# Performance work log

Hardware: AMD Instinct MI355X
Metric: run time of the kernel (lower is better)

The kernel has to match this reference:

```python
import jax, jax.numpy as jnp
import numpy as np

D = 256          # out_feats
H = 4            # n_heads
DH = D // H      # per-head feats
S = 8192         # number of snapshots (segments)
PER = 32         # edges (selected papers) per snapshot
E = S * PER      # total edges
NP = 200000      # number of papers
ST = 10          # snapshot_types (embedding has ST+1 rows, padding_idx=-1)
SLOPE = 0.01     # LeakyReLU negative slope (torch default)


def setup_inputs() -> dict:
    key = jax.random.key(0)
    ks = jax.random.split(key, 20)
    sc = 1.0 / np.sqrt(D)
    papers = jax.random.normal(ks[0], (NP, D), dtype=jnp.float32)
    snapshots = jax.random.normal(ks[1], (S, D), dtype=jnp.float32)
    cur_snapshot_types = jax.random.randint(ks[2], (S,), 0, ST + 1, dtype=jnp.int32)
    is_cite = jax.random.randint(ks[3], (NP,), 0, 2, dtype=jnp.int32)
    selected_indicator = jax.random.randint(ks[4], (E,), 0, NP, dtype=jnp.int64)
    # contiguous sorted segment ids, PER edges per snapshot (matches valid_num_nodes)
    index = jnp.repeat(jnp.arange(S, dtype=jnp.int32), PER)
    # linear layers (torch Linear: y = x @ W.T + b)
    W_src = jax.random.normal(ks[5], (D, D), dtype=jnp.float32) * sc
    b_src = jnp.zeros((D,), dtype=jnp.float32)
    W_dst = jax.random.normal(ks[6], (D, D), dtype=jnp.float32) * sc
    b_dst = jnp.zeros((D,), dtype=jnp.float32)
    W_out = jax.random.normal(ks[7], (D, D), dtype=jnp.float32) * sc
    b_out = jnp.zeros((D,), dtype=jnp.float32)
    # node attr embeddings (2 rows, padding_idx=0 -> row 0 zero)
    emb_cite = jax.random.normal(ks[8], (2, D), dtype=jnp.float32).at[0].set(0.0)
    emb_ref = jax.random.normal(ks[9], (2, D), dtype=jnp.float32).at[0].set(0.0)
    emb_target = jax.random.normal(ks[10], (2, D), dtype=jnp.float32).at[0].set(0.0)
    # snapshot type embedding (ST+1 rows, padding_idx=-1 -> last row zero)
    snapshot_emb = jax.random.normal(ks[11], (ST + 1, D), dtype=jnp.float32).at[-1].set(0.0)
    # attention vectors, xavier_normal with relu gain
    gain = np.sqrt(2.0)
    std = gain * np.sqrt(2.0 / (H * DH + 1))
    attn = jax.random.normal(ks[12], (1, H, DH), dtype=jnp.float32) * std
    attn_t = jax.random.normal(ks[13], (1, H, DH), dtype=jnp.float32) * std
    return {
        "papers": papers, "snapshots": snapshots,
        "W_src": W_src, "b_src": b_src, "W_dst": W_dst, "b_dst": b_dst,
        "W_out": W_out, "b_out": b_out,
        "emb_cite": emb_cite, "emb_ref": emb_ref, "emb_target": emb_target,
        "snapshot_emb": snapshot_emb, "attn": attn, "attn_t": attn_t,
        "cur_snapshot_types": cur_snapshot_types, "is_cite": is_cite,
        "selected_indicator": selected_indicator, "index": index,
    }


def _leaky(x):
    return jnp.where(x >= 0, x, SLOPE * x)


def reference(papers, snapshots, W_src, b_src, W_dst, b_dst, W_out, b_out,
              emb_cite, emb_ref, emb_target, snapshot_emb, attn, attn_t,
              cur_snapshot_types, is_cite, selected_indicator, index):
    # gather src papers per edge: [E, D]
    h_src = papers[selected_indicator]
    feat_src = (h_src @ W_src.T + b_src).reshape(-1, H, DH)          # [E,H,DH]
    ic = is_cite[selected_indicator]
    # original uses 'is_cite' indices for all three attr embeddings (faithful)
    src_type_h = (emb_cite[ic] + emb_ref[ic] + emb_target[ic]).reshape(-1, H, DH)
    dst_type_h = snapshot_emb[cur_snapshot_types].reshape(-1, H, DH)  # [S,H,DH]
    feat_dst = (snapshots @ W_dst.T + b_dst).reshape(-1, H, DH)[index]  # [E,H,DH]
    # per-edge attention logits
    e = (_leaky(feat_src + feat_dst) * attn).sum(axis=-1)             # [E,H]
    et = (_leaky(src_type_h + dst_type_h[index]) * attn_t).sum(axis=-1)
    e = e + et
    # segment (edge) softmax over destination snapshots
    m = jax.lax.stop_gradient(jax.ops.segment_max(e, index, num_segments=S))
    ex = jnp.exp(e - m[index])
    den = jax.ops.segment_sum(ex, index, num_segments=S)
    a = (ex / den[index])[..., None]                                  # [E,H,1]
    # weighted segment-sum aggregation
    x = feat_src * a
    sum_out = jax.ops.segment_sum(x, index, num_segments=S).reshape(S, D)
    return sum_out @ W_out.T + b_out
```

## Files before the change

### kernel.cpp

```cpp
#include <hip/hip_runtime.h>
#include <hip/hip_fp16.h>
#include <type_traits>

#define NSNAP 8192
#define PER 32
#define SLOPE 0.01f

using half8   = __attribute__((ext_vector_type(8))) _Float16;
using floatx4 = __attribute__((ext_vector_type(4))) float;

__device__ __forceinline__ float leaky(float x) { return x >= 0.f ? x : SLOPE * x; }

__device__ __forceinline__ unsigned pack2(float a, float b) {
    __half2 h = __floats2half2_rn(a, b);
    return *reinterpret_cast<unsigned*>(&h);
}

template <typename AT, typename OT, bool DO_PACK>
__global__ __launch_bounds__(256) void gemm64(const AT* __restrict__ A,
                                              const float* __restrict__ W,
                                              const float* __restrict__ bias,
                                              OT* __restrict__ Cout, int M,
                                              const float* __restrict__ Wsrc,
                                              _Float16* __restrict__ Wh) {
    if constexpr (DO_PACK) {
        if (blockIdx.y == 4) {
            if (blockIdx.x < 32) {
                const int t = blockIdx.x * 256 + threadIdx.x;
                const int lane = t & 63;
                const int wj = (t >> 6) & 15;
                const int k0 = t >> 10;
                const int n = (wj >> 2) * 64 + (wj & 3) * 16 + (lane & 15);
                const int k = k0 * 32 + (lane >> 4) * 8;
                const float4 v0 = *(const float4*)(Wsrc + (long)n * 256 + k);
                const float4 v1 = *(const float4*)(Wsrc + (long)n * 256 + k + 4);
                *(uint4*)(Wh + (long)t * 8) = make_uint4(pack2(v0.x, v0.y), pack2(v0.z, v0.w),
                                                         pack2(v1.x, v1.y), pack2(v1.z, v1.w));
            }
            return;
        }
    }
    constexpr int LDA = 40;
    __shared__ _Float16 Asl[64 * LDA];
    __shared__ _Float16 Wsl[64 * LDA];

    const int m0 = blockIdx.x * 64;
    const int n0 = blockIdx.y * 64;
    const int tid = threadIdx.x;
    const int lane = tid & 63;
    const int wave = tid >> 6;
    const int wm = (wave & 1) * 32;
    const int wn = (wave >> 1) * 32;
    const int l15 = lane & 15;
    const int quad = lane >> 4;

    floatx4 acc[2][2];
#pragma unroll
    for (int i = 0; i < 2; i++)
#pragma unroll
        for (int j = 0; j < 2; j++) acc[i][j] = (floatx4)0.f;

    for (int k0 = 0; k0 < 256; k0 += 32) {
        __syncthreads();
#pragma unroll
        for (int it = 0; it < 2; ++it) {
            const int idx = tid + it * 256;
            const int row = idx >> 3;
            const int c4 = idx & 7;
            if constexpr (std::is_same_v<AT, float>) {
                const float4 v = *(const float4*)(A + (long)(m0 + row) * 256 + k0 + c4 * 4);
                *(uint2*)(&Asl[row * LDA + c4 * 4]) = make_uint2(pack2(v.x, v.y), pack2(v.z, v.w));
            } else {
                const uint2 v = *(const uint2*)(A + (long)(m0 + row) * 256 + k0 + c4 * 4);
                *(uint2*)(&Asl[row * LDA + c4 * 4]) = v;
            }
            const float4 w = *(const float4*)(W + (long)(n0 + row) * 256 + k0 + c4 * 4);
            *(uint2*)(&Wsl[row * LDA + c4 * 4]) = make_uint2(pack2(w.x, w.y), pack2(w.z, w.w));
        }
        __syncthreads();

        half8 af[2], bf[2];
#pragma unroll
        for (int i = 0; i < 2; i++)
            af[i] = *reinterpret_cast<const half8*>(&Asl[(wm + i * 16 + l15) * LDA + quad * 8]);
#pragma unroll
        for (int j = 0; j < 2; j++)
            bf[j] = *reinterpret_cast<const half8*>(&Wsl[(wn + j * 16 + l15) * LDA + quad * 8]);
#pragma unroll
        for (int i = 0; i < 2; i++)
#pragma unroll
            for (int j = 0; j < 2; j++)
                acc[i][j] = __builtin_amdgcn_mfma_f32_16x16x32_f16(af[i], bf[j], acc[i][j], 0, 0, 0);
    }

#pragma unroll
    for (int j = 0; j < 2; j++) {
        const int gcol = n0 + wn + j * 16 + l15;
        const float bv = bias[gcol];
#pragma unroll
        for (int i = 0; i < 2; i++) {
            const int rbase = m0 + wm + i * 16 + quad * 4;
#pragma unroll
            for (int r = 0; r < 4; r++) {
                const float v = acc[i][j][r] + bv;
                if constexpr (std::is_same_v<OT, __half>)
                    Cout[(long)(rbase + r) * 256 + gcol] = __float2half(v);
                else
                    Cout[(long)(rbase + r) * 256 + gcol] = v;
            }
        }
    }
}

__global__ __launch_bounds__(256, 4) void fused_attn(
    const float* __restrict__ papers, const _Float16* __restrict__ Wh,
    const float* __restrict__ b_src, const float* __restrict__ F,
    const float* __restrict__ emb_cite, const float* __restrict__ emb_ref,
    const float* __restrict__ emb_target, const float* __restrict__ snap_emb,
    const float* __restrict__ attn, const float* __restrict__ attn_t,
    const int* __restrict__ types, const int* __restrict__ is_cite,
    const int* __restrict__ sel, __half* __restrict__ SO) {
    __shared__ _Float16 Asl[64 * 256];

    const int tid = threadIdx.x;
    const int lane = tid & 63;
    const int wave = tid >> 6;
    const int l15 = lane & 15;
    const int quad = lane >> 4;
    const int sbase = blockIdx.x * 2;
    const int ebase = blockIdx.x * 64;

    const int icv = is_cite[sel[ebase + lane]];
    const unsigned long long icmask = __ballot(icv != 0);

    {
        const int row = wave * 16 + l15;
        const long arow = (long)sel[ebase + row];
        const float* src = papers + arow * 256;
#pragma unroll
        for (int m = 0; m < 16; m++) {
            const float4 v = *(const float4*)(src + m * 16 + quad * 4);
            const int c8 = m * 2 + (quad >> 1);
            const int slot = (c8 >> 2) * 256 + wave * 64 + (c8 & 3) * 16 + l15;
            *(uint2*)(&Asl[slot * 8 + (quad & 1) * 4]) =
                make_uint2(pack2(v.x, v.y), pack2(v.z, v.w));
        }
    }
    __syncthreads();

    floatx4 acc[4][4];
#pragma unroll
    for (int i = 0; i < 4; i++)
#pragma unroll
        for (int j = 0; j < 4; j++) acc[i][j] = (floatx4)0.f;

    for (int k0 = 0; k0 < 8; k0++) {
        half8 af[4], bf[4];
#pragma unroll
        for (int i = 0; i < 4; i++)
            af[i] = *reinterpret_cast<const half8*>(&Asl[(k0 * 256 + i * 64 + lane) * 8]);
#pragma unroll
        for (int j = 0; j < 4; j++)
            bf[j] = *reinterpret_cast<const half8*>(Wh + ((k0 * 16 + wave * 4 + j) * 64 + lane) * 8);
#pragma unroll
        for (int i = 0; i < 4; i++)
#pragma unroll
            for (int j = 0; j < 4; j++)
                acc[i][j] = __builtin_amdgcn_mfma_f32_16x16x32_f16(af[i], bf[j], acc[i][j], 0, 0, 0);
    }

    float bsrc_j[4], attn_j[4], F0_j[4], F1_j[4];
#pragma unroll
    for (int j = 0; j < 4; j++) {
        const int col = 64 * wave + j * 16 + l15;
        bsrc_j[j] = b_src[col];
        attn_j[j] = attn[col];
        F0_j[j] = F[(long)sbase * 256 + col];
        F1_j[j] = F[(long)(sbase + 1) * 256 + col];
    }
#pragma unroll
    for (int i = 0; i < 4; i++)
#pragma unroll
        for (int j = 0; j < 4; j++)
#pragma unroll
            for (int r = 0; r < 4; r++) acc[i][j][r] += bsrc_j[j];

    const int D = 64 * wave + lane;
    const float at_d = attn_t[D];
    const float src0 = emb_cite[D] + emb_ref[D] + emb_target[D];
    const float src1 = emb_cite[256 + D] + emb_ref[256 + D] + emb_target[256 + D];
    float et[2][2];
#pragma unroll
    for (int sn = 0; sn < 2; sn++) {
        const float dstt = snap_emb[types[sbase + sn] * 256 + D];
        float p0 = leaky(src0 + dstt) * at_d;
        float p1 = leaky(src1 + dstt) * at_d;
#pragma unroll
        for (int off = 32; off; off >>= 1) {
            p0 += __shfl_xor(p0, off);
            p1 += __shfl_xor(p1, off);
        }
        et[sn][0] = p0;
        et[sn][1] = p1;
    }

    float lg[4][4];
#pragma unroll
    for (int i = 0; i < 4; i++) {
        const int sn = i >> 1;
#pragma unroll
        for (int r = 0; r < 4; r++) {
            float p = 0.f;
#pragma unroll
            for (int j = 0; j < 4; j++)
                p += leaky(acc[i][j][r] + (sn == 0 ? F0_j[j] : F1_j[j])) * attn_j[j];
#pragma unroll
            for (int off = 1; off <= 8; off <<= 1) p += __shfl_xor(p, off);
            const int row = i * 16 + quad * 4 + r;
            lg[i][r] = p + (((icmask >> row) & 1ull) ? et[sn][1] : et[sn][0]);
        }
    }

    float aw[4][4];
#pragma unroll
    for (int sn = 0; sn < 2; sn++) {
        float m = -3.4e38f;
#pragma unroll
        for (int ii = 0; ii < 2; ii++)
#pragma unroll
            for (int r = 0; r < 4; r++) m = fmaxf(m, lg[sn * 2 + ii][r]);
        m = fmaxf(m, __shfl_xor(m, 16));
        m = fmaxf(m, __shfl_xor(m, 32));
        float den = 0.f;
#pragma unroll
        for (int ii = 0; ii < 2; ii++)
#pragma unroll
            for (int r = 0; r < 4; r++) {
                const float ex = __expf(lg[sn * 2 + ii][r] - m);
                aw[sn * 2 + ii][r] = ex;
                den += ex;
            }
        den += __shfl_xor(den, 16);
        den += __shfl_xor(den, 32);
        const float inv = 1.f / den;
#pragma unroll
        for (int ii = 0; ii < 2; ii++)
#pragma unroll
            for (int r = 0; r < 4; r++) aw[sn * 2 + ii][r] *= inv;
    }

#pragma unroll
    for (int sn = 0; sn < 2; sn++) {
#pragma unroll
        for (int j = 0; j < 4; j++) {
            float o = 0.f;
#pragma unroll
            for (int ii = 0; ii < 2; ii++)
#pragma unroll
                for (int r = 0; r < 4; r++) o += aw[sn * 2 + ii][r] * acc[sn * 2 + ii][j][r];
            o += __shfl_xor(o, 16);
            o += __shfl_xor(o, 32);
            if (quad == sn)
                SO[(long)(sbase + sn) * 256 + 64 * wave + j * 16 + l15] = __float2half(o);
        }
    }
}

extern "C" void kernel_launch(void* const* d_in, const int* in_sizes, int n_in,
                              void* d_out, int out_size, void* d_ws, size_t ws_size,
                              hipStream_t stream) {
    const float* papers     = (const float*)d_in[0];
    const float* snapshots  = (const float*)d_in[1];
    const float* W_src      = (const float*)d_in[2];
    const float* b_src      = (const float*)d_in[3];
    const float* W_dst      = (const float*)d_in[4];
    const float* b_dst      = (const float*)d_in[5];
    const float* W_out      = (const float*)d_in[6];
    const float* b_out      = (const float*)d_in[7];
    const float* emb_cite   = (const float*)d_in[8];
    const float* emb_ref    = (const float*)d_in[9];
    const float* emb_target = (const float*)d_in[10];
    const float* snap_emb   = (const float*)d_in[11];
    const float* attn       = (const float*)d_in[12];
    const float* attn_t     = (const float*)d_in[13];
    const int* types        = (const int*)d_in[14];
    const int* is_cite      = (const int*)d_in[15];
    const int* sel          = (const int*)d_in[16];

    char* ws = (char*)d_ws;
    float*     F    = (float*)ws;
    __half*    SO   = (__half*)(ws + 8388608);
    _Float16*  Wh   = (_Float16*)(ws + 12582912);

    gemm64<float, float, true><<<dim3(128, 5), 256, 0, stream>>>(snapshots, W_dst, b_dst, F,
                                                                 NSNAP, W_src, Wh);
    fused_attn<<<NSNAP / 2, 256, 0, stream>>>(papers, Wh, b_src, F, emb_cite, emb_ref,
                                              emb_target, snap_emb, attn, attn_t, types,
                                              is_cite, sel, SO);
    gemm64<__half, float, false><<<dim3(128, 4), 256, 0, stream>>>(SO, W_out, b_out,
                                                                   (float*)d_out, NSNAP,
                                                                   nullptr, nullptr);
}
```

Measured before the change: 385.3 us.

## Software-pipeline paper gathers across four snapshots per block with double-buffered LDS

Each block of the fused attention kernel now handles four snapshots one at a time instead of two at once. While the MFMA and softmax work runs on the current snapshot, the gathered paper rows for the next snapshot are loaded into registers and then written into a second LDS buffer. The aim is to hide the latency of the random global gathers behind compute. The costs are more registers (launch bounds lowered to 3 blocks per SM), half as many blocks, and one barrier per snapshot.

Result: slower. 409.7 us (+6.4%).

```diff
diff --git a/kernel.cpp b/kernel.cpp
--- a/kernel.cpp
+++ b/kernel.cpp
@@ -112,7 +112,7 @@
     }
 }
 
-__global__ __launch_bounds__(256, 4) void fused_attn(
+__global__ __launch_bounds__(256, 3) void fused_attn(
     const float* __restrict__ papers, const _Float16* __restrict__ Wh,
     const float* __restrict__ b_src, const float* __restrict__ F,
     const float* __restrict__ emb_cite, const float* __restrict__ emb_ref,
@@ -120,149 +120,178 @@
     const float* __restrict__ attn, const float* __restrict__ attn_t,
     const int* __restrict__ types, const int* __restrict__ is_cite,
     const int* __restrict__ sel, __half* __restrict__ SO) {
-    __shared__ _Float16 Asl[64 * 256];
+    __shared__ _Float16 Asl[2][8192];
 
     const int tid = threadIdx.x;
     const int lane = tid & 63;
     const int wave = tid >> 6;
     const int l15 = lane & 15;
     const int quad = lane >> 4;
-    const int sbase = blockIdx.x * 2;
-    const int ebase = blockIdx.x * 64;
-
-    const int icv = is_cite[sel[ebase + lane]];
-    const unsigned long long icmask = __ballot(icv != 0);
-
-    {
-        const int row = wave * 16 + l15;
-        const long arow = (long)sel[ebase + row];
-        const float* src = papers + arow * 256;
-#pragma unroll
-        for (int m = 0; m < 16; m++) {
-            const float4 v = *(const float4*)(src + m * 16 + quad * 4);
-            const int c8 = m * 2 + (quad >> 1);
-            const int slot = (c8 >> 2) * 256 + wave * 64 + (c8 & 3) * 16 + l15;
-            *(uint2*)(&Asl[slot * 8 + (quad & 1) * 4]) =
-                make_uint2(pack2(v.x, v.y), pack2(v.z, v.w));
-        }
-    }
-    __syncthreads();
-
-    floatx4 acc[4][4];
-#pragma unroll
-    for (int i = 0; i < 4; i++)
-#pragma unroll
-        for (int j = 0; j < 4; j++) acc[i][j] = (floatx4)0.f;
-
-    for (int k0 = 0; k0 < 8; k0++) {
-        half8 af[4], bf[4];
-#pragma unroll
-        for (int i = 0; i < 4; i++)
-            af[i] = *reinterpret_cast<const half8*>(&Asl[(k0 * 256 + i * 64 + lane) * 8]);
-#pragma unroll
-        for (int j = 0; j < 4; j++)
-            bf[j] = *reinterpret_cast<const half8*>(Wh + ((k0 * 16 + wave * 4 + j) * 64 + lane) * 8);
-#pragma unroll
-        for (int i = 0; i < 4; i++)
-#pragma unroll
-            for (int j = 0; j < 4; j++)
-                acc[i][j] = __builtin_amdgcn_mfma_f32_16x16x32_f16(af[i], bf[j], acc[i][j], 0, 0, 0);
-    }
-
-    float bsrc_j[4], attn_j[4], F0_j[4], F1_j[4];
+    const int grow = tid >> 3;
+    const int gc = tid & 7;
+    const int s0 = blockIdx.x * 4;
+
+    float bsrc_j[4], attn_j[4];
 #pragma unroll
     for (int j = 0; j < 4; j++) {
         const int col = 64 * wave + j * 16 + l15;
         bsrc_j[j] = b_src[col];
         attn_j[j] = attn[col];
-        F0_j[j] = F[(long)sbase * 256 + col];
-        F1_j[j] = F[(long)(sbase + 1) * 256 + col];
-    }
-#pragma unroll
-    for (int i = 0; i < 4; i++)
-#pragma unroll
-        for (int j = 0; j < 4; j++)
-#pragma unroll
-            for (int r = 0; r < 4; r++) acc[i][j][r] += bsrc_j[j];
-
+    }
     const int D = 64 * wave + lane;
     const float at_d = attn_t[D];
     const float src0 = emb_cite[D] + emb_ref[D] + emb_target[D];
     const float src1 = emb_cite[256 + D] + emb_ref[256 + D] + emb_target[256 + D];
-    float et[2][2];
-#pragma unroll
-    for (int sn = 0; sn < 2; sn++) {
-        const float dstt = snap_emb[types[sbase + sn] * 256 + D];
-        float p0 = leaky(src0 + dstt) * at_d;
-        float p1 = leaky(src1 + dstt) * at_d;
-#pragma unroll
-        for (int off = 32; off; off >>= 1) {
-            p0 += __shfl_xor(p0, off);
-            p1 += __shfl_xor(p1, off);
-        }
-        et[sn][0] = p0;
-        et[sn][1] = p1;
-    }
-
-    float lg[4][4];
-#pragma unroll
-    for (int i = 0; i < 4; i++) {
-        const int sn = i >> 1;
-#pragma unroll
-        for (int r = 0; r < 4; r++) {
-            float p = 0.f;
+
+    int selrow = sel[s0 * 32 + grow];
+    int selic = sel[s0 * 32 + (lane & 31)];
+    float4 g[8];
+    {
+        const float* sp = papers + (long)selrow * 256;
+#pragma unroll
+        for (int m = 0; m < 8; m++) g[m] = *(const float4*)(sp + m * 32 + gc * 4);
+    }
+    int icv = is_cite[selic];
+    int typ = types[s0];
+    int selrow_n = sel[(s0 + 1) * 32 + grow];
+    int selic_n = sel[(s0 + 1) * 32 + (lane & 31)];
+    int typ_n = types[s0 + 1];
+
+#pragma unroll
+    for (int p = 0; p < 4; p++) {
+#pragma unroll
+        for (int m = 0; m < 8; m++) {
+            const int c8 = m * 4 + (gc >> 1);
+            const int slot = (c8 >> 2) * 128 + (grow >> 4) * 64 + (c8 & 3) * 16 + (grow & 15);
+            *(uint2*)(&Asl[p & 1][slot * 8 + (gc & 1) * 4]) =
+                make_uint2(pack2(g[m].x, g[m].y), pack2(g[m].z, g[m].w));
+        }
+        __syncthreads();
+
+        if (p < 3) {
+            const float* sp = papers + (long)selrow_n * 256;
+#pragma unroll
+            for (int m = 0; m < 8; m++) g[m] = *(const float4*)(sp + m * 32 + gc * 4);
+        }
+        int icv_n = 0;
+        if (p < 3) icv_n = is_cite[selic_n];
+        int selrow_n2 = 0, selic_n2 = 0, typ_n2 = 0;
+        if (p < 2) {
+            selrow_n2 = sel[(s0 + p + 2) * 32 + grow];
+            selic_n2 = sel[(s0 + p + 2) * 32 + (lane & 31)];
+            typ_n2 = types[s0 + p + 2];
+        }
+        float F_j[4];
+#pragma unroll
+        for (int j = 0; j < 4; j++)
+            F_j[j] = F[(long)(s0 + p) * 256 + 64 * wave + j * 16 + l15];
+        const float dstt = snap_emb[typ * 256 + D];
+
+        floatx4 acc[2][4];
+#pragma unroll
+        for (int i = 0; i < 2; i++)
+#pragma unroll
+            for (int j = 0; j < 4; j++) acc[i][j] = (floatx4)0.f;
+#pragma unroll
+        for (int k0 = 0; k0 < 8; k0++) {
+            half8 af[2], bf[4];
+#pragma unroll
+            for (int i = 0; i < 2; i++)
+                af[i] = *reinterpret_cast<const half8*>(
+                    &Asl[p & 1][(k0 * 128 + i * 64 + quad * 16 + l15) * 8]);
 #pragma unroll
             for (int j = 0; j < 4; j++)
-                p += leaky(acc[i][j][r] + (sn == 0 ? F0_j[j] : F1_j[j])) * attn_j[j];
-#pragma unroll
-            for (int off = 1; off <= 8; off <<= 1) p += __shfl_xor(p, off);
-            const int row = i * 16 + quad * 4 + r;
-            lg[i][r] = p + (((icmask >> row) & 1ull) ? et[sn][1] : et[sn][0]);
-        }
-    }
-
-    float aw[4][4];
-#pragma unroll
-    for (int sn = 0; sn < 2; sn++) {
-        float m = -3.4e38f;
-#pragma unroll
-        for (int ii = 0; ii < 2; ii++)
-#pragma unroll
-            for (int r = 0; r < 4; r++) m = fmaxf(m, lg[sn * 2 + ii][r]);
-        m = fmaxf(m, __shfl_xor(m, 16));
-        m = fmaxf(m, __shfl_xor(m, 32));
-        float den = 0.f;
-#pragma unroll
-        for (int ii = 0; ii < 2; ii++)
+                bf[j] = *reinterpret_cast<const half8*>(
+                    Wh + ((k0 * 16 + wave * 4 + j) * 64 + lane) * 8);
+#pragma unroll
+            for (int i = 0; i < 2; i++)
+#pragma unroll
+                for (int j = 0; j < 4; j++)
+                    acc[i][j] =
+                        __builtin_amdgcn_mfma_f32_16x16x32_f16(af[i], bf[j], acc[i][j], 0, 0, 0);
+        }
+
+#pragma unroll
+        for (int i = 0; i < 2; i++)
+#pragma unroll
+            for (int j = 0; j < 4; j++)
+#pragma unroll
+                for (int r = 0; r < 4; r++) acc[i][j][r] += bsrc_j[j];
+
+        const unsigned long long icmask = __ballot(icv != 0);
+        float et0, et1;
+        {
+            float p0 = leaky(src0 + dstt) * at_d;
+            float p1 = leaky(src1 + dstt) * at_d;
+#pragma unroll
+            for (int off = 32; off; off >>= 1) {
+                p0 += __shfl_xor(p0, off);
+                p1 += __shfl_xor(p1, off);
+            }
+            et0 = p0;
+            et1 = p1;
+        }
+
+        float lg[2][4];
+#pragma unroll
+        for (int i = 0; i < 2; i++) {
 #pragma unroll
             for (int r = 0; r < 4; r++) {
-                const float ex = __expf(lg[sn * 2 + ii][r] - m);
-                aw[sn * 2 + ii][r] = ex;
-                den += ex;
-            }
-        den += __shfl_xor(den, 16);
-        den += __shfl_xor(den, 32);
-        const float inv = 1.f / den;
-#pragma unroll
-        for (int ii = 0; ii < 2; ii++)
-#pragma unroll
-            for (int r = 0; r < 4; r++) aw[sn * 2 + ii][r] *= inv;
-    }
-
-#pragma unroll
-    for (int sn = 0; sn < 2; sn++) {
+                float pv = 0.f;
+#pragma unroll
+                for (int j = 0; j < 4; j++) pv += leaky(acc[i][j][r] + F_j[j]) * attn_j[j];
+#pragma unroll
+                for (int off = 1; off <= 8; off <<= 1) pv += __shfl_xor(pv, off);
+                const int row = i * 16 + quad * 4 + r;
+                lg[i][r] = pv + (((icmask >> row) & 1ull) ? et1 : et0);
+            }
+        }
+
+        float aw[2][4];
+        {
+            float mx = -3.4e38f;
+#pragma unroll
+            for (int i = 0; i < 2; i++)
+#pragma unroll
+                for (int r = 0; r < 4; r++) mx = fmaxf(mx, lg[i][r]);
+            mx = fmaxf(mx, __shfl_xor(mx, 16));
+            mx = fmaxf(mx, __shfl_xor(mx, 32));
+            float den = 0.f;
+#pragma unroll
+            for (int i = 0; i < 2; i++)
+#pragma unroll
+                for (int r = 0; r < 4; r++) {
+                    const float ex = __expf(lg[i][r] - mx);
+                    aw[i][r] = ex;
+                    den += ex;
+                }
+            den += __shfl_xor(den, 16);
+            den += __shfl_xor(den, 32);
+            const float inv = 1.f / den;
+#pragma unroll
+            for (int i = 0; i < 2; i++)
+#pragma unroll
+                for (int r = 0; r < 4; r++) aw[i][r] *= inv;
+        }
+
 #pragma unroll
         for (int j = 0; j < 4; j++) {
             float o = 0.f;
 #pragma unroll
-            for (int ii = 0; ii < 2; ii++)
-#pragma unroll
-                for (int r = 0; r < 4; r++) o += aw[sn * 2 + ii][r] * acc[sn * 2 + ii][j][r];
+            for (int i = 0; i < 2; i++)
+#pragma unroll
+                for (int r = 0; r < 4; r++) o += aw[i][r] * acc[i][j][r];
             o += __shfl_xor(o, 16);
             o += __shfl_xor(o, 32);
-            if (quad == sn)
-                SO[(long)(sbase + sn) * 256 + 64 * wave + j * 16 + l15] = __float2half(o);
-        }
+            if (quad == 0)
+                SO[(long)(s0 + p) * 256 + 64 * wave + j * 16 + l15] = __float2half(o);
+        }
+
+        icv = icv_n;
+        selrow_n = selrow_n2;
+        selic_n = selic_n2;
+        typ = typ_n;
+        typ_n = typ_n2;
     }
 }
 
@@ -294,7 +323,7 @@
 
     gemm64<float, float, true><<<dim3(128, 5), 256, 0, stream>>>(snapshots, W_dst, b_dst, F,
                                                                  NSNAP, W_src, Wh);
-    fused_attn<<<NSNAP / 2, 256, 0, stream>>>(papers, Wh, b_src, F, emb_cite, emb_ref,
+    fused_attn<<<NSNAP / 4, 256, 0, stream>>>(papers, Wh, b_src, F, emb_cite, emb_ref,
                                               emb_target, snap_emb, attn, attn_t, types,
                                               is_cite, sel, SO);
     gemm64<__half, float, false><<<dim3(128, 4), 256, 0, stream>>>(SO, W_out, b_out,
```
